# Optimization experiments

Measured on AMD Instinct MI355X. Metric: run time of the kernel, lower is better.

The kernel has to match this reference:

```python
import jax, jax.numpy as jnp
import numpy as np

B, T, S, C, H = 2, 2048, 2048, 1024, 16
D = C // H  # head dim = 64


def setup_inputs() -> dict:
    key = jax.random.key(0)
    ks = jax.random.split(key, 6)
    sc = 1.0 / np.sqrt(C)
    return {
        "q": jax.random.normal(ks[0], (B, T, C), jnp.float32),
        "p": jax.random.normal(ks[1], (B, S, C), jnp.float32),
        "Wq": jax.random.normal(ks[2], (C, C), jnp.float32) * sc,
        "Wk": jax.random.normal(ks[3], (C, C), jnp.float32) * sc,
        "Wv": jax.random.normal(ks[4], (C, C), jnp.float32) * sc,
        "Wo": jax.random.normal(ks[5], (C, C), jnp.float32) * sc,
    }


def reference(q, p, Wq, Wk, Wv, Wo):
    # Linear projections (no bias: config.bias=True -> nn.Linear bias=False)
    qh = (q @ Wq).reshape(B, T, H, D)  # [B,T,H,D]
    kh = (p @ Wk).reshape(B, S, H, D)  # [B,S,H,D]
    vh = (p @ Wv).reshape(B, S, H, D)  # [B,S,H,D]
    scale = 1.0 / jnp.sqrt(jnp.asarray(D, qh.dtype))
    att = jnp.einsum('bthd,bshd->bhts', qh, kh) * scale  # [B,H,T,S]
    att = jax.nn.softmax(att, axis=-1)
    y = jnp.einsum('bhts,bshd->bthd', att, vh).reshape(B, T, C)
    y = y @ Wo  # c_proj, dropout p=0 (eval)
    return y
```

## Files before the change

### kernel.cpp

```cpp
#include <hip/hip_runtime.h>
#include <hip/hip_bf16.h>
#include <stdint.h>

#define T_LEN 2048
#define CDIM  1024

typedef short bf16x8_t  __attribute__((ext_vector_type(8)));
typedef float f32x4_t   __attribute__((ext_vector_type(4)));
typedef float f32x16_t  __attribute__((ext_vector_type(16)));

__device__ __forceinline__ void gload_lds16(const void* gptr, void* lptr) {
  __builtin_amdgcn_global_load_lds(
      (const __attribute__((address_space(1))) unsigned int*)(gptr),
      (__attribute__((address_space(3))) unsigned int*)(lptr),
      16, 0, 0);
}

__device__ __forceinline__ unsigned short f2bf(float f) {
  union { float f; unsigned int u; } v; v.f = f;
  unsigned int u = v.u;
  return (unsigned short)((u + 0x7fffu + ((u >> 16) & 1u)) >> 16);
}

__device__ __forceinline__ unsigned int pk_bf16(float lo, float hi) {
  unsigned int r;
  asm("v_cvt_pk_bf16_f32 %0, %1, %2" : "=v"(r) : "v"(lo), "v"(hi));
  return r;
}
__device__ __forceinline__ unsigned short bf1(float v) {
  return (unsigned short)pk_bf16(v, v);
}

__global__ __launch_bounds__(256) void cast2_f32_bf16(const float* __restrict__ x0,
                                                      const float* __restrict__ x1,
                                                      unsigned short* __restrict__ y0,
                                                      unsigned short* __restrict__ y1) {
  int i = blockIdx.x * 256 + threadIdx.x;
  const float* x = blockIdx.y ? x1 : x0;
  unsigned short* y = blockIdx.y ? y1 : y0;
  const float4* x4 = (const float4*)x;
  float4 a = x4[i * 2], b = x4[i * 2 + 1];
  union { unsigned short u[8]; uint4 v; } o;
  o.u[0] = f2bf(a.x); o.u[1] = f2bf(a.y); o.u[2] = f2bf(a.z); o.u[3] = f2bf(a.w);
  o.u[4] = f2bf(b.x); o.u[5] = f2bf(b.y); o.u[6] = f2bf(b.z); o.u[7] = f2bf(b.w);
  ((uint4*)y)[i] = o.v;
}

__global__ __launch_bounds__(256) void transpose_cast4(const float* __restrict__ W0,
                                                       const float* __restrict__ W1,
                                                       const float* __restrict__ W2,
                                                       const float* __restrict__ W3,
                                                       unsigned short* __restrict__ Wall,
                                                       unsigned short* __restrict__ Wot) {
  __shared__ float tile[32][33];
  int z = blockIdx.z;
  const float* W = (z == 0) ? W0 : (z == 1) ? W1 : (z == 2) ? W2 : W3;
  unsigned short* Wt = (z < 3) ? (Wall + (size_t)z * 1024 * 1024) : Wot;
  int tx = threadIdx.x & 31, ty = threadIdx.x >> 5;
  int n0 = blockIdx.x * 32, k0 = blockIdx.y * 32;
#pragma unroll
  for (int i = 0; i < 4; ++i) {
    int r = ty + i * 8;
    tile[r][tx] = W[(size_t)(k0 + r) * CDIM + n0 + tx];
  }
  __syncthreads();
#pragma unroll
  for (int i = 0; i < 4; ++i) {
    int r = ty + i * 8;
    Wt[(size_t)(n0 + r) * CDIM + k0 + tx] = f2bf(tile[tx][r]);
  }
}

__global__ __launch_bounds__(256) void gemm_qkv(const unsigned short* __restrict__ qbm,
                                                const unsigned short* __restrict__ pbm,
                                                const unsigned short* __restrict__ Wall,
                                                unsigned short* __restrict__ Qh,
                                                unsigned short* __restrict__ Kh,
                                                unsigned short* __restrict__ Vt) {
  __shared__ unsigned short ldsA[2][128 * 64];
  __shared__ unsigned short ldsB[2][128 * 64];
  const int tid = threadIdx.x, lane = tid & 63, w = tid >> 6;
  const int wr = w >> 1, wc = w & 1;
  const int nblk = blockIdx.x % 24, mblk = blockIdx.x / 24;
  const int m0 = mblk * 128;
  const int n0 = nblk * 128;
  const char* Ab = (const char*)((nblk < 8) ? qbm : pbm);
  const char* Bb = (const char*)Wall;
  f32x4_t acc[4][4] = {};

  auto stage = [&](int buf, int kt) {
#pragma unroll
    for (int it = 0; it < 4; ++it) {
      int ob = it * 4096 + w * 1024;
      int o = ob + lane * 16;
      int row = o >> 7, cin = o & 127;
      int cs = cin ^ ((row & 7) << 4);
      gload_lds16(Ab + (size_t)(m0 + row) * 2048 + kt * 128 + cs, (char*)ldsA[buf] + ob);
      gload_lds16(Bb + (size_t)(n0 + row) * 2048 + kt * 128 + cs, (char*)ldsB[buf] + ob);
    }
  };

  stage(0, 0);
  __syncthreads();
  int cur = 0;
  for (int kt = 0; kt < 16; ++kt) {
    if (kt < 15) stage(cur ^ 1, kt + 1);
    const char* lA = (const char*)ldsA[cur];
    const char* lB = (const char*)ldsB[cur];
#pragma unroll
    for (int kf = 0; kf < 2; ++kf) {
      int c = kf * 64 + ((lane >> 4) << 4);
      bf16x8_t af[4], bfr[4];
#pragma unroll
      for (int mf = 0; mf < 4; ++mf) {
        int row = wr * 64 + mf * 16 + (lane & 15);
        af[mf] = *(const bf16x8_t*)(lA + row * 128 + (c ^ ((row & 7) << 4)));
      }
#pragma unroll
      for (int nf = 0; nf < 4; ++nf) {
        int row = wc * 64 + nf * 16 + (lane & 15);
        bfr[nf] = *(const bf16x8_t*)(lB + row * 128 + (c ^ ((row & 7) << 4)));
      }
      __builtin_amdgcn_s_setprio(1);
#pragma unroll
      for (int mf = 0; mf < 4; ++mf)
#pragma unroll
        for (int nf = 0; nf < 4; ++nf)
          acc[mf][nf] = __builtin_amdgcn_mfma_f32_16x16x32_bf16(af[mf], bfr[nf], acc[mf][nf], 0, 0, 0);
      __builtin_amdgcn_s_setprio(0);
    }
    __syncthreads();
    cur ^= 1;
  }

  const float oscale = (nblk < 8) ? 0.18033688011112042f : 1.0f;
#pragma unroll
  for (int mf = 0; mf < 4; ++mf)
#pragma unroll
    for (int nf = 0; nf < 4; ++nf)
#pragma unroll
      for (int j = 0; j < 4; ++j) {
        int row = m0 + wr * 64 + mf * 16 + ((lane >> 4) << 2) + j;
        int col = n0 + wc * 64 + nf * 16 + (lane & 15);
        float v = acc[mf][nf][j] * oscale;
        int b = row >> 11, ts = row & 2047;
        if (col < 1024) {
          int h = col >> 6, d = col & 63;
          Qh[(((size_t)(b * 16 + h)) * 2048 + ts) * 64 + d] = bf1(v);
        } else if (col < 2048) {
          int cc = col - 1024, h = cc >> 6, d = cc & 63;
          Kh[(((size_t)(b * 16 + h)) * 2048 + ts) * 64 + d] = bf1(v);
        } else {
          int cc = col - 2048, h = cc >> 6, d = cc & 63;
          Vt[(((size_t)(b * 16 + h)) * 64 + d) * 2048 + ts] = bf1(v);
        }
      }
}

__global__ __launch_bounds__(256) void gemm_out(const unsigned short* __restrict__ A,
                                                const unsigned short* __restrict__ Bt,
                                                float* __restrict__ Out) {
  __shared__ unsigned short ldsA[2][128 * 64];
  __shared__ unsigned short ldsB[2][64 * 64];
  const int tid = threadIdx.x, lane = tid & 63, w = tid >> 6;
  const int m0 = (blockIdx.x >> 4) * 128;
  const int n0 = (blockIdx.x & 15) * 64;
  const char* Ab = (const char*)A;
  const char* Bb = (const char*)Bt;
  f32x4_t acc[2][4] = {};

  auto stage = [&](int buf, int kt) {
#pragma unroll
    for (int it = 0; it < 4; ++it) {
      int ob = it * 4096 + w * 1024;
      int o = ob + lane * 16;
      int row = o >> 7, cin = o & 127;
      int cs = cin ^ ((row & 7) << 4);
      gload_lds16(Ab + (size_t)(m0 + row) * 2048 + kt * 128 + cs, (char*)ldsA[buf] + ob);
    }
#pragma unroll
    for (int it = 0; it < 2; ++it) {
      int ob = it * 4096 + w * 1024;
      int o = ob + lane * 16;
      int row = o >> 7, cin = o & 127;
      int cs = cin ^ ((row & 7) << 4);
      gload_lds16(Bb + (size_t)(n0 + row) * 2048 + kt * 128 + cs, (char*)ldsB[buf] + ob);
    }
  };

  stage(0, 0);
  __syncthreads();
  int cur = 0;
  for (int kt = 0; kt < 16; ++kt) {
    if (kt < 15) stage(cur ^ 1, kt + 1);
    const char* lA = (const char*)ldsA[cur];
    const char* lB = (const char*)ldsB[cur];
#pragma unroll
    for (int kf = 0; kf < 2; ++kf) {
      int c = kf * 64 + ((lane >> 4) << 4);
      bf16x8_t af[2], bfr[4];
#pragma unroll
      for (int mf = 0; mf < 2; ++mf) {
        int row = w * 32 + mf * 16 + (lane & 15);
        af[mf] = *(const bf16x8_t*)(lA + row * 128 + (c ^ ((row & 7) << 4)));
      }
#pragma unroll
      for (int nf = 0; nf < 4; ++nf) {
        int row = nf * 16 + (lane & 15);
        bfr[nf] = *(const bf16x8_t*)(lB + row * 128 + (c ^ ((row & 7) << 4)));
      }
      __builtin_amdgcn_s_setprio(1);
#pragma unroll
      for (int mf = 0; mf < 2; ++mf)
#pragma unroll
        for (int nf = 0; nf < 4; ++nf)
          acc[mf][nf] = __builtin_amdgcn_mfma_f32_16x16x32_bf16(af[mf], bfr[nf], acc[mf][nf], 0, 0, 0);
      __builtin_amdgcn_s_setprio(0);
    }
    __syncthreads();
    cur ^= 1;
  }

#pragma unroll
  for (int mf = 0; mf < 2; ++mf)
#pragma unroll
    for (int nf = 0; nf < 4; ++nf)
#pragma unroll
      for (int j = 0; j < 4; ++j) {
        int row = m0 + w * 32 + mf * 16 + ((lane >> 4) << 2) + j;
        int col = n0 + nf * 16 + (lane & 15);
        Out[(size_t)row * 1024 + col] = acc[mf][nf][j];
      }
}

__global__ __launch_bounds__(256) void attn32(const unsigned short* __restrict__ Qg,
                                              const unsigned short* __restrict__ Kg,
                                              const unsigned short* __restrict__ Vtg,
                                              unsigned short* __restrict__ Ag) {
  __shared__ unsigned short ldsK[2][64 * 64];
  __shared__ unsigned short ldsV[2][64 * 64];
  const int tid = threadIdx.x, lane = tid & 63, w = tid >> 6;
  const int hi = lane >> 5, ql = lane & 31;
  const int bh = blockIdx.y;
  const int q0 = blockIdx.x * 128 + w * 32;

  bf16x8_t qf[4];
#pragma unroll
  for (int kd = 0; kd < 4; ++kd)
    qf[kd] = *(const bf16x8_t*)(Qg + ((size_t)bh * T_LEN + q0 + ql) * 64 + kd * 16 + hi * 8);

  bf16x8_t ones;
#pragma unroll
  for (int i = 0; i < 8; ++i) ones[i] = (short)0x3F80;

  f32x16_t oacc[2] = {};
  f32x16_t lacc = {};

  const char* Kb = (const char*)(Kg + (size_t)bh * 2048 * 64);
  const char* Vb = (const char*)(Vtg + (size_t)bh * 64 * 2048);

  auto stage = [&](int buf, int s0) {
#pragma unroll
    for (int it = 0; it < 2; ++it) {
      int ob = it * 4096 + w * 1024;
      int o = ob + lane * 16;
      int row = o >> 7, cin = o & 127;
      int cs = cin ^ ((row & 7) << 4);
      gload_lds16(Kb + (size_t)s0 * 128 + row * 128 + cs, (char*)ldsK[buf] + ob);
      gload_lds16(Vb + (size_t)s0 * 2 + (size_t)row * 4096 + cs, (char*)ldsV[buf] + ob);
    }
  };

  stage(0, 0);
  __syncthreads();
  int cur = 0;

  for (int s0 = 0; s0 < 2048; s0 += 64) {
    if (s0 + 64 < 2048) stage(cur ^ 1, s0 + 64);
    const char* lK = (const char*)ldsK[cur];
    const char* lV = (const char*)ldsV[cur];

    f32x16_t sacc[2] = {};
    __builtin_amdgcn_s_setprio(1);
#pragma unroll
    for (int sub = 0; sub < 2; ++sub) {
      int row = sub * 32 + ql;
      int swz = (row & 7) << 4;
#pragma unroll
      for (int kd = 0; kd < 4; ++kd) {
        bf16x8_t kfrag = *(const bf16x8_t*)(lK + row * 128 + ((kd * 32 + hi * 16) ^ swz));
        sacc[sub] = __builtin_amdgcn_mfma_f32_32x32x16_bf16(kfrag, qf[kd], sacc[sub], 0, 0, 0);
      }
    }
    __builtin_amdgcn_s_setprio(0);

#pragma unroll
    for (int sub = 0; sub < 2; ++sub)
#pragma unroll
      for (int r = 0; r < 16; ++r) sacc[sub][r] = exp2f(sacc[sub][r]);

#pragma unroll
    for (int ks = 0; ks < 4; ++ks) {
      const int sub = ks >> 1, mA = (ks & 1) * 2, mB = mA + 1;
      unsigned int a0 = pk_bf16(sacc[sub][4 * mA + 0], sacc[sub][4 * mA + 1]);
      unsigned int a1 = pk_bf16(sacc[sub][4 * mA + 2], sacc[sub][4 * mA + 3]);
      unsigned int b0 = pk_bf16(sacc[sub][4 * mB + 0], sacc[sub][4 * mB + 1]);
      unsigned int b1 = pk_bf16(sacc[sub][4 * mB + 2], sacc[sub][4 * mB + 3]);
      asm("v_permlane32_swap_b32 %0, %1" : "+v"(a0), "+v"(b0));
      asm("v_permlane32_swap_b32 %0, %1" : "+v"(a1), "+v"(b1));
      union { unsigned int u[4]; bf16x8_t v; } P;
      P.u[0] = a0; P.u[1] = a1; P.u[2] = b0; P.u[3] = b1;
      __builtin_amdgcn_s_setprio(1);
      lacc = __builtin_amdgcn_mfma_f32_32x32x16_bf16(P.v, ones, lacc, 0, 0, 0);
#pragma unroll
      for (int dt = 0; dt < 2; ++dt) {
        int row = dt * 32 + ql;
        bf16x8_t vfrag = *(const bf16x8_t*)(lV + row * 128 + ((ks * 32 + hi * 16) ^ ((row & 7) << 4)));
        oacc[dt] = __builtin_amdgcn_mfma_f32_32x32x16_bf16(P.v, vfrag, oacc[dt], 0, 0, 0);
      }
      __builtin_amdgcn_s_setprio(0);
    }
    __syncthreads();
    cur ^= 1;
  }

  const int b = bh >> 4, h = bh & 15;
#pragma unroll
  for (int grp = 0; grp < 4; ++grp)
#pragma unroll
    for (int r2 = 0; r2 < 4; ++r2) {
      int reg = grp * 4 + r2;
      float linv = 1.0f / lacc[reg];
      int t = q0 + 4 * hi + 8 * grp + r2;
#pragma unroll
      for (int dt = 0; dt < 2; ++dt) {
        int col = h * 64 + dt * 32 + ql;
        float v = oacc[dt][reg] * linv;
        Ag[((size_t)b * T_LEN + t) * CDIM + col] = bf1(v);
      }
    }
}

extern "C" void kernel_launch(void* const* d_in, const int* in_sizes, int n_in,
                              void* d_out, int out_size, void* d_ws, size_t ws_size,
                              hipStream_t stream) {
  const float* q  = (const float*)d_in[0];
  const float* p  = (const float*)d_in[1];
  const float* Wq = (const float*)d_in[2];
  const float* Wk = (const float*)d_in[3];
  const float* Wv = (const float*)d_in[4];
  const float* Wo = (const float*)d_in[5];

  char* ws = (char*)d_ws;
  unsigned short* qb   = (unsigned short*)(ws);
  unsigned short* pb   = (unsigned short*)(ws + ((size_t)8 << 20));
  unsigned short* Wall = (unsigned short*)(ws + ((size_t)16 << 20));
  unsigned short* Wot  = (unsigned short*)(ws + ((size_t)22 << 20));
  unsigned short* Qh   = (unsigned short*)(ws + ((size_t)24 << 20));
  unsigned short* Kh   = (unsigned short*)(ws + ((size_t)32 << 20));
  unsigned short* Vt   = (unsigned short*)(ws + ((size_t)40 << 20));
  unsigned short* Ao   = (unsigned short*)(ws + ((size_t)48 << 20));

  cast2_f32_bf16<<<dim3(2048, 2), 256, 0, stream>>>(q, p, qb, pb);
  transpose_cast4<<<dim3(32, 32, 4), 256, 0, stream>>>(Wq, Wk, Wv, Wo, Wall, Wot);

  gemm_qkv<<<768, 256, 0, stream>>>(qb, pb, Wall, Qh, Kh, Vt);

  attn32<<<dim3(16, 32), 256, 0, stream>>>(Qh, Kh, Vt, Ao);

  gemm_out<<<512, 256, 0, stream>>>(Ao, Wot, (float*)d_out);
}
```

Measured before the change: 156.9 us.

## Split attention over the key dimension into two halves and add a combine kernel

The attention kernel becomes a template with a SPLIT parameter. With SPLIT=2 each block processes half of the key/value sequence and writes unnormalized fp32 partial outputs plus row sums to workspace. A new combine kernel adds the two halves, normalizes, and writes bf16. The goal is to double the number of blocks for better occupancy and latency hiding, at the cost of about 64MB of extra fp32 traffic and one more kernel launch. The exp2 call is also switched to the amdgcn builtin when it is available.

```diff
diff --git a/kernel.cpp b/kernel.cpp
--- a/kernel.cpp
+++ b/kernel.cpp
@@ -8,6 +8,12 @@
 typedef short bf16x8_t  __attribute__((ext_vector_type(8)));
 typedef float f32x4_t   __attribute__((ext_vector_type(4)));
 typedef float f32x16_t  __attribute__((ext_vector_type(16)));
+
+#if __has_builtin(__builtin_amdgcn_exp2f)
+#define EXP2(x) __builtin_amdgcn_exp2f(x)
+#else
+#define EXP2(x) exp2f(x)
+#endif
 
 __device__ __forceinline__ void gload_lds16(const void* gptr, void* lptr) {
   __builtin_amdgcn_global_load_lds(
@@ -233,16 +239,22 @@
       }
 }
 
+template <int SPLIT>
 __global__ __launch_bounds__(256) void attn32(const unsigned short* __restrict__ Qg,
                                               const unsigned short* __restrict__ Kg,
                                               const unsigned short* __restrict__ Vtg,
-                                              unsigned short* __restrict__ Ag) {
+                                              unsigned short* __restrict__ Ag,
+                                              float* __restrict__ O0,
+                                              float* __restrict__ O1,
+                                              float* __restrict__ Lp) {
   __shared__ unsigned short ldsK[2][64 * 64];
   __shared__ unsigned short ldsV[2][64 * 64];
   const int tid = threadIdx.x, lane = tid & 63, w = tid >> 6;
   const int hi = lane >> 5, ql = lane & 31;
   const int bh = blockIdx.y;
   const int q0 = blockIdx.x * 128 + w * 32;
+  const int z = (SPLIT == 2) ? blockIdx.z : 0;
+  const int sBeg = z * (2048 / SPLIT), sEnd = sBeg + 2048 / SPLIT;
 
   bf16x8_t qf[4];
 #pragma unroll
@@ -271,12 +283,12 @@
     }
   };
 
-  stage(0, 0);
+  stage(0, sBeg);
   __syncthreads();
   int cur = 0;
 
-  for (int s0 = 0; s0 < 2048; s0 += 64) {
-    if (s0 + 64 < 2048) stage(cur ^ 1, s0 + 64);
+  for (int s0 = sBeg; s0 < sEnd; s0 += 64) {
+    if (s0 + 64 < sEnd) stage(cur ^ 1, s0 + 64);
     const char* lK = (const char*)ldsK[cur];
     const char* lV = (const char*)ldsV[cur];
 
@@ -297,7 +309,7 @@
 #pragma unroll
     for (int sub = 0; sub < 2; ++sub)
 #pragma unroll
-      for (int r = 0; r < 16; ++r) sacc[sub][r] = exp2f(sacc[sub][r]);
+      for (int r = 0; r < 16; ++r) sacc[sub][r] = EXP2(sacc[sub][r]);
 
 #pragma unroll
     for (int ks = 0; ks < 4; ++ks) {
@@ -325,20 +337,60 @@
   }
 
   const int b = bh >> 4, h = bh & 15;
-#pragma unroll
-  for (int grp = 0; grp < 4; ++grp)
-#pragma unroll
-    for (int r2 = 0; r2 < 4; ++r2) {
-      int reg = grp * 4 + r2;
-      float linv = 1.0f / lacc[reg];
-      int t = q0 + 4 * hi + 8 * grp + r2;
-#pragma unroll
-      for (int dt = 0; dt < 2; ++dt) {
-        int col = h * 64 + dt * 32 + ql;
-        float v = oacc[dt][reg] * linv;
-        Ag[((size_t)b * T_LEN + t) * CDIM + col] = bf1(v);
-      }
-    }
+  if (SPLIT == 1) {
+#pragma unroll
+    for (int grp = 0; grp < 4; ++grp)
+#pragma unroll
+      for (int r2 = 0; r2 < 4; ++r2) {
+        int reg = grp * 4 + r2;
+        float linv = 1.0f / lacc[reg];
+        int t = q0 + 4 * hi + 8 * grp + r2;
+#pragma unroll
+        for (int dt = 0; dt < 2; ++dt) {
+          int col = h * 64 + dt * 32 + ql;
+          float v = oacc[dt][reg] * linv;
+          Ag[((size_t)b * T_LEN + t) * CDIM + col] = bf1(v);
+        }
+      }
+  } else {
+    float* Op = z ? O1 : O0;
+#pragma unroll
+    for (int grp = 0; grp < 4; ++grp)
+#pragma unroll
+      for (int r2 = 0; r2 < 4; ++r2) {
+        int reg = grp * 4 + r2;
+        int t = q0 + 4 * hi + 8 * grp + r2;
+#pragma unroll
+        for (int dt = 0; dt < 2; ++dt)
+          Op[((size_t)b * T_LEN + t) * CDIM + h * 64 + dt * 32 + ql] = oacc[dt][reg];
+        if (ql == 0)
+          Lp[(((size_t)z * 2 + b) * 16 + h) * T_LEN + t] = lacc[reg];
+      }
+  }
+}
+
+__global__ __launch_bounds__(256) void attn_combine(const float* __restrict__ O0,
+                                                    const float* __restrict__ O1,
+                                                    const float* __restrict__ Lp,
+                                                    unsigned short* __restrict__ Ag) {
+  int i = blockIdx.x * 256 + threadIdx.x;
+  int c8 = i & 127, bt = i >> 7;
+  int b = bt >> 11, t = bt & 2047;
+  int c = c8 * 8, h = c >> 6;
+  float l0 = Lp[(((size_t)0 * 2 + b) * 16 + h) * T_LEN + t];
+  float l1 = Lp[(((size_t)1 * 2 + b) * 16 + h) * T_LEN + t];
+  float inv = 1.0f / (l0 + l1);
+  size_t off = (size_t)bt * CDIM + c;
+  float4 x0 = *(const float4*)(O0 + off);
+  float4 x1 = *(const float4*)(O1 + off);
+  float4 y0 = *(const float4*)(O0 + off + 4);
+  float4 y1 = *(const float4*)(O1 + off + 4);
+  union { unsigned int u[4]; uint4 v; } o;
+  o.u[0] = pk_bf16((x0.x + x1.x) * inv, (x0.y + x1.y) * inv);
+  o.u[1] = pk_bf16((x0.z + x1.z) * inv, (x0.w + x1.w) * inv);
+  o.u[2] = pk_bf16((y0.x + y1.x) * inv, (y0.y + y1.y) * inv);
+  o.u[3] = pk_bf16((y0.z + y1.z) * inv, (y0.w + y1.w) * inv);
+  *(uint4*)(Ag + off) = o.v;
 }
 
 extern "C" void kernel_launch(void* const* d_in, const int* in_sizes, int n_in,
@@ -360,13 +412,22 @@
   unsigned short* Kh   = (unsigned short*)(ws + ((size_t)32 << 20));
   unsigned short* Vt   = (unsigned short*)(ws + ((size_t)40 << 20));
   unsigned short* Ao   = (unsigned short*)(ws + ((size_t)48 << 20));
+  float* O0 = (float*)(ws);
+  float* O1 = (float*)(ws + ((size_t)56 << 20));
+  float* Lp = (float*)(ws + ((size_t)72 << 20));
 
   cast2_f32_bf16<<<dim3(2048, 2), 256, 0, stream>>>(q, p, qb, pb);
   transpose_cast4<<<dim3(32, 32, 4), 256, 0, stream>>>(Wq, Wk, Wv, Wo, Wall, Wot);
 
   gemm_qkv<<<768, 256, 0, stream>>>(qb, pb, Wall, Qh, Kh, Vt);
 
-  attn32<<<dim3(16, 32), 256, 0, stream>>>(Qh, Kh, Vt, Ao);
+  const size_t needed = ((size_t)72 << 20) + ((size_t)1 << 19);
+  if (ws_size >= needed) {
+    attn32<2><<<dim3(16, 32, 2), 256, 0, stream>>>(Qh, Kh, Vt, nullptr, O0, O1, Lp);
+    attn_combine<<<2048, 256, 0, stream>>>(O0, O1, Lp, Ao);
+  } else {
+    attn32<1><<<dim3(16, 32, 1), 256, 0, stream>>>(Qh, Kh, Vt, Ao, nullptr, nullptr, nullptr);
+  }
 
   gemm_out<<<512, 256, 0, stream>>>(Ao, Wot, (float*)d_out);
 }
```

New measurement: 150.2 us. 4.3% less time.
